# Kernel tuning notes

Measured on AMD Instinct MI355X. Metric: run time of the kernel, lower is better.

## Reference

```python
import jax, jax.numpy as jnp
import numpy as np

N_NODES = 16384
N_EDGES = 8192
D_FEAT = 64


def setup_inputs() -> dict:
    key = jax.random.key(0)
    k1, k2 = jax.random.split(key)
    incidence_matrix = jax.random.uniform(k1, (N_NODES, N_EDGES), dtype=jnp.float32)
    features = jax.random.normal(k2, (N_NODES, D_FEAT), dtype=jnp.float32)
    return {"incidence_matrix": incidence_matrix, "features": features}


def reference(incidence_matrix, features):
    # Faithful to the original: compute_degree_matrices returns RAW degree
    # diagonals (no inversion despite variable names). torch.diag(d) @ X is
    # exactly a row-broadcast scaling d[:, None] * X.
    d_v = jnp.sum(incidence_matrix, axis=1)  # [N] node degrees
    d_e = jnp.sum(incidence_matrix, axis=0)  # [M] hyperedge degrees
    X = features * d_v[:, None]                       # D_v @ X        [N, d]
    X_hyperedge = incidence_matrix.T @ X              # H^T @ X        [M, d]
    X_hyperedge = X_hyperedge * d_e[:, None]          # D_e @ (.)      [M, d]
    X = incidence_matrix @ X_hyperedge                # H @ (.)        [N, d]
    X = X * d_v[:, None]                              # D_v @ (.)      [N, d]
    return X
```

## Files before the change

kernel.cpp:

```cpp
#include <hip/hip_runtime.h>

#define N_NODES 16384
#define N_EDGES 8192
#define D_FEAT  64


__global__ __launch_bounds__(256, 4) void dvscale_kernel(const float* __restrict__ H,
                                                         const float* __restrict__ F,
                                                         float* __restrict__ dv,
                                                         float* __restrict__ Xs) {
    const int wave = threadIdx.x >> 6;
    const int lane = threadIdx.x & 63;
    const int n = blockIdx.x * 4 + wave;
    const float4* row = (const float4*)(H + (size_t)n * N_EDGES);
    float s = 0.f;
#pragma unroll
    for (int j = 0; j < 32; ++j) {
        float4 v = row[lane + 64 * j];
        s += v.x + v.y + v.z + v.w;
    }
#pragma unroll
    for (int off = 32; off > 0; off >>= 1) s += __shfl_down(s, off, 64);
    s = __shfl(s, 0, 64);
    if (lane == 0) dv[n] = s;
    Xs[(size_t)n * D_FEAT + lane] = F[(size_t)n * D_FEAT + lane] * s;
}

__global__ __launch_bounds__(256, 4) void gemm1_kernel(const float* __restrict__ H,
                                                       const float* __restrict__ Xs,
                                                       float* __restrict__ Y,
                                                       float* __restrict__ de) {
    const int et = blockIdx.x & 127;
    const int ks = blockIdx.x >> 7;
    const int e0 = et * 64;
    const int kbeg = ks * 2048;
    const int kend = kbeg + 2048;

    __shared__ float Hs[32 * 68];
    __shared__ float Xt[32 * 68];

    const int t = threadIdx.x;
    const int r  = t >> 4;
    const int c4 = (t & 15) * 4;
    const int eg = (t & 15) * 4;
    const int dg = (t >> 4) * 4;

    float acc[4][4] = {};
    float dea[4] = {0.f, 0.f, 0.f, 0.f};

    for (int k0 = kbeg; k0 < kend; k0 += 32) {
        __syncthreads();
#pragma unroll
        for (int i = 0; i < 2; ++i) {
            const int rr = r + 16 * i;
            float4 h = *(const float4*)(H + (size_t)(k0 + rr) * N_EDGES + e0 + c4);
            *(float4*)(Hs + rr * 68 + c4) = h;
            dea[0] += h.x; dea[1] += h.y; dea[2] += h.z; dea[3] += h.w;
            float4 x = *(const float4*)(Xs + (size_t)(k0 + rr) * D_FEAT + c4);
            *(float4*)(Xt + rr * 68 + c4) = x;
        }
        __syncthreads();
#pragma unroll 8
        for (int k = 0; k < 32; ++k) {
            float4 h = *(const float4*)(Hs + k * 68 + eg);
            float4 x = *(const float4*)(Xt + k * 68 + dg);
            acc[0][0] += h.x * x.x; acc[0][1] += h.x * x.y; acc[0][2] += h.x * x.z; acc[0][3] += h.x * x.w;
            acc[1][0] += h.y * x.x; acc[1][1] += h.y * x.y; acc[1][2] += h.y * x.z; acc[1][3] += h.y * x.w;
            acc[2][0] += h.z * x.x; acc[2][1] += h.z * x.y; acc[2][2] += h.z * x.z; acc[2][3] += h.z * x.w;
            acc[3][0] += h.w * x.x; acc[3][1] += h.w * x.y; acc[3][2] += h.w * x.z; acc[3][3] += h.w * x.w;
        }
    }

#pragma unroll
    for (int i = 0; i < 4; ++i)
#pragma unroll
        for (int j = 0; j < 4; ++j)
            atomicAdd(&Y[(size_t)(e0 + eg + i) * D_FEAT + dg + j], acc[i][j]);
#pragma unroll
    for (int j = 0; j < 4; ++j) atomicAdd(&de[e0 + c4 + j], dea[j]);
}

__global__ __launch_bounds__(256) void scaley_kernel(float* __restrict__ Y,
                                                     const float* __restrict__ de) {
    const int idx = blockIdx.x * 256 + threadIdx.x;
    const int e = idx >> 4;
    const float d = de[e];
    float4 v = ((float4*)Y)[idx];
    v.x *= d; v.y *= d; v.z *= d; v.w *= d;
    ((float4*)Y)[idx] = v;
}

__global__ __launch_bounds__(256, 4) void gemm2_kernel(const float* __restrict__ H,
                                                       const float* __restrict__ Y,
                                                       float* __restrict__ Yacc) {
    const int mt = blockIdx.x & 255;
    const int ks = blockIdx.x >> 8;
    const int m0 = mt * 64;
    const int kbeg = ks * 2048;
    const int kend = kbeg + 2048;

    __shared__ float Hst[32 * 68];
    __shared__ float Yt[32 * 68];

    const int t = threadIdx.x;
    const int mg = (t & 15) * 4;
    const int dg = (t >> 4) * 4;

    float acc[4][4] = {};

    for (int k0 = kbeg; k0 < kend; k0 += 32) {
        __syncthreads();
#pragma unroll
        for (int i = 0; i < 2; ++i) {
            const int idx = t + 256 * i;
            const int m = idx >> 3;
            const int k4 = (idx & 7) * 4;
            float4 h = *(const float4*)(H + (size_t)(m0 + m) * N_EDGES + k0 + k4);
            Hst[(k4 + 0) * 68 + m] = h.x;
            Hst[(k4 + 1) * 68 + m] = h.y;
            Hst[(k4 + 2) * 68 + m] = h.z;
            Hst[(k4 + 3) * 68 + m] = h.w;
            const int rr = idx >> 4;
            const int c4 = (idx & 15) * 4;
            float4 y = *(const float4*)(Y + (size_t)(k0 + rr) * D_FEAT + c4);
            *(float4*)(Yt + rr * 68 + c4) = y;
        }
        __syncthreads();
#pragma unroll 8
        for (int k = 0; k < 32; ++k) {
            float4 h = *(const float4*)(Hst + k * 68 + mg);
            float4 x = *(const float4*)(Yt + k * 68 + dg);
            acc[0][0] += h.x * x.x; acc[0][1] += h.x * x.y; acc[0][2] += h.x * x.z; acc[0][3] += h.x * x.w;
            acc[1][0] += h.y * x.x; acc[1][1] += h.y * x.y; acc[1][2] += h.y * x.z; acc[1][3] += h.y * x.w;
            acc[2][0] += h.z * x.x; acc[2][1] += h.z * x.y; acc[2][2] += h.z * x.z; acc[2][3] += h.z * x.w;
            acc[3][0] += h.w * x.x; acc[3][1] += h.w * x.y; acc[3][2] += h.w * x.z; acc[3][3] += h.w * x.w;
        }
    }

#pragma unroll
    for (int i = 0; i < 4; ++i)
#pragma unroll
        for (int j = 0; j < 4; ++j)
            atomicAdd(&Yacc[(size_t)(m0 + mg + i) * D_FEAT + dg + j], acc[i][j]);
}

__global__ __launch_bounds__(256) void scaleout_kernel(const float* __restrict__ Yacc,
                                                       const float* __restrict__ dv,
                                                       float* __restrict__ out) {
    const int idx = blockIdx.x * 256 + threadIdx.x;
    const int n = idx >> 4;
    const float d = dv[n];
    float4 v = ((const float4*)Yacc)[idx];
    v.x *= d; v.y *= d; v.z *= d; v.w *= d;
    ((float4*)out)[idx] = v;
}

extern "C" void kernel_launch(void* const* d_in, const int* in_sizes, int n_in,
                              void* d_out, int out_size, void* d_ws, size_t ws_size,
                              hipStream_t stream) {
    const float* H = (const float*)d_in[0];
    const float* F = (const float*)d_in[1];
    float* out = (float*)d_out;
    float* ws = (float*)d_ws;

    float* dv   = ws;
    float* de   = ws + 16384;
    float* Xs   = ws + 24576;
    float* Y    = ws + 24576 + N_NODES * D_FEAT;
    float* Yacc = Y + N_EDGES * D_FEAT;

    hipMemsetAsync(de, 0, N_EDGES * sizeof(float), stream);
    hipMemsetAsync(Y, 0, (size_t)N_EDGES * D_FEAT * sizeof(float), stream);
    hipMemsetAsync(Yacc, 0, (size_t)N_NODES * D_FEAT * sizeof(float), stream);

    dvscale_kernel<<<N_NODES / 4, 256, 0, stream>>>(H, F, dv, Xs);
    gemm1_kernel<<<1024, 256, 0, stream>>>(H, Xs, Y, de);
    scaley_kernel<<<(N_EDGES * D_FEAT / 4) / 256, 256, 0, stream>>>(Y, de);
    gemm2_kernel<<<1024, 256, 0, stream>>>(H, Y, Yacc);
    scaleout_kernel<<<(N_NODES * D_FEAT / 4) / 256, 256, 0, stream>>>(Yacc, dv, out);
}
```

Baseline: 1.228 ms.

## Convert H to bf16 once and run both GEMMs on bf16 MFMA

The degree pass now also writes a bf16 copy of the incidence matrix. Both GEMMs then read this half-size copy and use MFMA 16x16x32 bf16 instructions with swizzled LDS tiles, replacing the fp32 FMA loops. A transpose kernel makes the scaled features and the intermediate K-contiguous bf16, so the MFMA operands can be loaded directly. This removes fp32 scalar compute and halves H traffic in the GEMMs, at the cost of one extra bf16 write of H and a loss of precision that could exceed the harness tolerance. The edge degrees are now summed from the bf16-rounded values.

```diff
diff --git a/kernel.cpp b/kernel.cpp
--- a/kernel.cpp
+++ b/kernel.cpp
@@ -4,20 +4,38 @@
 #define N_EDGES 8192
 #define D_FEAT  64
 
-
-__global__ __launch_bounds__(256, 4) void dvscale_kernel(const float* __restrict__ H,
-                                                         const float* __restrict__ F,
-                                                         float* __restrict__ dv,
-                                                         float* __restrict__ Xs) {
+typedef __attribute__((ext_vector_type(8))) short short8;
+typedef __attribute__((ext_vector_type(4))) float floatx4;
+
+__device__ __forceinline__ unsigned short f2bf(float f) {
+    unsigned int u = __float_as_uint(f);
+    return (unsigned short)((u + 0x7fffu + ((u >> 16) & 1u)) >> 16);
+}
+
+__device__ __forceinline__ int sw(int row, int g) {
+    return row * 32 + (g ^ (((row >> 3) & 7) * 4));
+}
+
+__global__ __launch_bounds__(256) void dvscale_kernel(const float* __restrict__ H,
+                                                      const float* __restrict__ F,
+                                                      float* __restrict__ dv,
+                                                      unsigned short* __restrict__ Hbf,
+                                                      float* __restrict__ Xs) {
     const int wave = threadIdx.x >> 6;
     const int lane = threadIdx.x & 63;
     const int n = blockIdx.x * 4 + wave;
     const float4* row = (const float4*)(H + (size_t)n * N_EDGES);
+    unsigned short* hrow = Hbf + (size_t)n * N_EDGES;
     float s = 0.f;
 #pragma unroll
     for (int j = 0; j < 32; ++j) {
         float4 v = row[lane + 64 * j];
         s += v.x + v.y + v.z + v.w;
+        unsigned long long pk = (unsigned long long)f2bf(v.x)
+                              | ((unsigned long long)f2bf(v.y) << 16)
+                              | ((unsigned long long)f2bf(v.z) << 32)
+                              | ((unsigned long long)f2bf(v.w) << 48);
+        *(unsigned long long*)(hrow + 4 * (lane + 64 * j)) = pk;
     }
 #pragma unroll
     for (int off = 32; off > 0; off >>= 1) s += __shfl_down(s, off, 64);
@@ -26,131 +44,207 @@
     Xs[(size_t)n * D_FEAT + lane] = F[(size_t)n * D_FEAT + lane] * s;
 }
 
-__global__ __launch_bounds__(256, 4) void gemm1_kernel(const float* __restrict__ H,
-                                                       const float* __restrict__ Xs,
-                                                       float* __restrict__ Y,
-                                                       float* __restrict__ de) {
-    const int et = blockIdx.x & 127;
-    const int ks = blockIdx.x >> 7;
-    const int e0 = et * 64;
-    const int kbeg = ks * 2048;
-    const int kend = kbeg + 2048;
-
-    __shared__ float Hs[32 * 68];
-    __shared__ float Xt[32 * 68];
-
+__global__ __launch_bounds__(256) void xst_kernel(const float* __restrict__ Xs,
+                                                  unsigned short* __restrict__ XsT) {
+    __shared__ float tile[64][65];
+    const int n0 = blockIdx.x * 64;
     const int t = threadIdx.x;
-    const int r  = t >> 4;
-    const int c4 = (t & 15) * 4;
-    const int eg = (t & 15) * 4;
-    const int dg = (t >> 4) * 4;
-
-    float acc[4][4] = {};
-    float dea[4] = {0.f, 0.f, 0.f, 0.f};
-
-    for (int k0 = kbeg; k0 < kend; k0 += 32) {
-        __syncthreads();
-#pragma unroll
-        for (int i = 0; i < 2; ++i) {
-            const int rr = r + 16 * i;
-            float4 h = *(const float4*)(H + (size_t)(k0 + rr) * N_EDGES + e0 + c4);
-            *(float4*)(Hs + rr * 68 + c4) = h;
-            dea[0] += h.x; dea[1] += h.y; dea[2] += h.z; dea[3] += h.w;
-            float4 x = *(const float4*)(Xs + (size_t)(k0 + rr) * D_FEAT + c4);
-            *(float4*)(Xt + rr * 68 + c4) = x;
-        }
-        __syncthreads();
-#pragma unroll 8
-        for (int k = 0; k < 32; ++k) {
-            float4 h = *(const float4*)(Hs + k * 68 + eg);
-            float4 x = *(const float4*)(Xt + k * 68 + dg);
-            acc[0][0] += h.x * x.x; acc[0][1] += h.x * x.y; acc[0][2] += h.x * x.z; acc[0][3] += h.x * x.w;
-            acc[1][0] += h.y * x.x; acc[1][1] += h.y * x.y; acc[1][2] += h.y * x.z; acc[1][3] += h.y * x.w;
-            acc[2][0] += h.z * x.x; acc[2][1] += h.z * x.y; acc[2][2] += h.z * x.z; acc[2][3] += h.z * x.w;
-            acc[3][0] += h.w * x.x; acc[3][1] += h.w * x.y; acc[3][2] += h.w * x.z; acc[3][3] += h.w * x.w;
-        }
-    }
-
-#pragma unroll
-    for (int i = 0; i < 4; ++i)
+    const int r = t >> 4, c4 = t & 15;
+#pragma unroll
+    for (int li = 0; li < 4; ++li) {
+        const int rr = r + 16 * li;
+        float4 v = *(const float4*)(Xs + (size_t)(n0 + rr) * 64 + c4 * 4);
+        tile[rr][c4 * 4 + 0] = v.x; tile[rr][c4 * 4 + 1] = v.y;
+        tile[rr][c4 * 4 + 2] = v.z; tile[rr][c4 * 4 + 3] = v.w;
+    }
+    __syncthreads();
+#pragma unroll
+    for (int li = 0; li < 4; ++li) {
+        const int d = r + 16 * li;
+        unsigned long long pk = (unsigned long long)f2bf(tile[c4 * 4 + 0][d])
+                              | ((unsigned long long)f2bf(tile[c4 * 4 + 1][d]) << 16)
+                              | ((unsigned long long)f2bf(tile[c4 * 4 + 2][d]) << 32)
+                              | ((unsigned long long)f2bf(tile[c4 * 4 + 3][d]) << 48);
+        *(unsigned long long*)(XsT + (size_t)d * N_NODES + n0 + c4 * 4) = pk;
+    }
+}
+
+__global__ __launch_bounds__(256) void gemm1_kernel(const unsigned short* __restrict__ Hbf,
+                                                    const unsigned short* __restrict__ XsT,
+                                                    float* __restrict__ YaccT,
+                                                    float* __restrict__ de) {
+    __shared__ unsigned int A32[128 * 32];
+    __shared__ unsigned int B32[64 * 32];
+    const int t = threadIdx.x;
+    const int w = t >> 6;
+    const int lane = t & 63;
+    const int e0 = (blockIdx.x & 63) * 128;
+    const int k0base = (blockIdx.x >> 6) * 1024;
+
+    const int seg = t & 15;
+    const int p = t >> 4;
+    const int bd = t >> 3;
+    const int bseg = t & 7;
+
+    floatx4 acc[2][4];
+#pragma unroll
+    for (int i = 0; i < 2; ++i)
+#pragma unroll
+        for (int j = 0; j < 4; ++j) acc[i][j] = (floatx4){0.f, 0.f, 0.f, 0.f};
+    float dea[8] = {0.f, 0.f, 0.f, 0.f, 0.f, 0.f, 0.f, 0.f};
+
+    for (int it = 0; it < 16; ++it) {
+        const int k0 = k0base + it * 64;
+        __syncthreads();
+#pragma unroll
+        for (int pp = 0; pp < 2; ++pp) {
+            const int pr = p + 16 * pp;
+            const unsigned short* src = Hbf + (size_t)(k0 + 2 * pr) * N_EDGES + e0 + seg * 8;
+            short8 r0 = *(const short8*)src;
+            short8 r1 = *(const short8*)(src + N_EDGES);
+#pragma unroll
+            for (int j = 0; j < 8; ++j) {
+                unsigned int lo = (unsigned short)r0[j];
+                unsigned int hi = (unsigned short)r1[j];
+                unsigned int pk = lo | (hi << 16);
+                const int e = seg * 8 + j;
+                A32[sw(e, pr & ~3) + (pr & 3)] = pk;
+                dea[j] += __uint_as_float(pk << 16) + __uint_as_float(pk & 0xffff0000u);
+            }
+        }
+#pragma unroll
+        for (int bb = 0; bb < 2; ++bb) {
+            const int d = bd + 32 * bb;
+            uint4 v = *(const uint4*)(XsT + (size_t)d * N_NODES + k0 + bseg * 8);
+            *(uint4*)&B32[sw(d, bseg * 4)] = v;
+        }
+        __syncthreads();
+#pragma unroll
+        for (int s = 0; s < 2; ++s) {
+            const int g = s * 16 + (lane >> 4) * 4;
+            short8 af[2];
+#pragma unroll
+            for (int i = 0; i < 2; ++i) {
+                const int row = 32 * w + 16 * i + (lane & 15);
+                af[i] = *(short8*)&A32[sw(row, g)];
+            }
+#pragma unroll
+            for (int j = 0; j < 4; ++j) {
+                const int row = 16 * j + (lane & 15);
+                short8 bf = *(short8*)&B32[sw(row, g)];
+#pragma unroll
+                for (int i = 0; i < 2; ++i)
+                    acc[i][j] = __builtin_amdgcn_mfma_f32_16x16x32_bf16(af[i], bf, acc[i][j], 0, 0, 0);
+            }
+        }
+    }
+
+#pragma unroll
+    for (int i = 0; i < 2; ++i)
 #pragma unroll
         for (int j = 0; j < 4; ++j)
-            atomicAdd(&Y[(size_t)(e0 + eg + i) * D_FEAT + dg + j], acc[i][j]);
-#pragma unroll
-    for (int j = 0; j < 4; ++j) atomicAdd(&de[e0 + c4 + j], dea[j]);
-}
-
-__global__ __launch_bounds__(256) void scaley_kernel(float* __restrict__ Y,
-                                                     const float* __restrict__ de) {
+#pragma unroll
+            for (int r = 0; r < 4; ++r) {
+                const int e = e0 + 32 * w + 16 * i + (lane >> 4) * 4 + r;
+                const int d = 16 * j + (lane & 15);
+                atomicAdd(&YaccT[(size_t)d * N_EDGES + e], acc[i][j][r]);
+            }
+#pragma unroll
+    for (int j = 0; j < 8; ++j) atomicAdd(&de[e0 + seg * 8 + j], dea[j]);
+}
+
+__global__ __launch_bounds__(256) void scaley_kernel(const float* __restrict__ YaccT,
+                                                     const float* __restrict__ de,
+                                                     unsigned short* __restrict__ Yt) {
     const int idx = blockIdx.x * 256 + threadIdx.x;
-    const int e = idx >> 4;
-    const float d = de[e];
-    float4 v = ((float4*)Y)[idx];
-    v.x *= d; v.y *= d; v.z *= d; v.w *= d;
-    ((float4*)Y)[idx] = v;
-}
-
-__global__ __launch_bounds__(256, 4) void gemm2_kernel(const float* __restrict__ H,
-                                                       const float* __restrict__ Y,
-                                                       float* __restrict__ Yacc) {
-    const int mt = blockIdx.x & 255;
-    const int ks = blockIdx.x >> 8;
-    const int m0 = mt * 64;
-    const int kbeg = ks * 2048;
-    const int kend = kbeg + 2048;
-
-    __shared__ float Hst[32 * 68];
-    __shared__ float Yt[32 * 68];
-
+    const int d = idx >> 11;
+    const int e4 = idx & 2047;
+    float4 y = ((const float4*)YaccT)[idx];
+    float4 sc = ((const float4*)de)[e4];
+    unsigned long long pk = (unsigned long long)f2bf(y.x * sc.x)
+                          | ((unsigned long long)f2bf(y.y * sc.y) << 16)
+                          | ((unsigned long long)f2bf(y.z * sc.z) << 32)
+                          | ((unsigned long long)f2bf(y.w * sc.w) << 48);
+    *(unsigned long long*)(Yt + (size_t)d * N_EDGES + e4 * 4) = pk;
+}
+
+__global__ __launch_bounds__(256) void gemm2_kernel(const unsigned short* __restrict__ Hbf,
+                                                    const unsigned short* __restrict__ Yt,
+                                                    float* __restrict__ OutAcc) {
+    __shared__ unsigned int A32[128 * 32];
+    __shared__ unsigned int B32[64 * 32];
     const int t = threadIdx.x;
-    const int mg = (t & 15) * 4;
-    const int dg = (t >> 4) * 4;
-
-    float acc[4][4] = {};
-
-    for (int k0 = kbeg; k0 < kend; k0 += 32) {
-        __syncthreads();
-#pragma unroll
-        for (int i = 0; i < 2; ++i) {
-            const int idx = t + 256 * i;
-            const int m = idx >> 3;
-            const int k4 = (idx & 7) * 4;
-            float4 h = *(const float4*)(H + (size_t)(m0 + m) * N_EDGES + k0 + k4);
-            Hst[(k4 + 0) * 68 + m] = h.x;
-            Hst[(k4 + 1) * 68 + m] = h.y;
-            Hst[(k4 + 2) * 68 + m] = h.z;
-            Hst[(k4 + 3) * 68 + m] = h.w;
-            const int rr = idx >> 4;
-            const int c4 = (idx & 15) * 4;
-            float4 y = *(const float4*)(Y + (size_t)(k0 + rr) * D_FEAT + c4);
-            *(float4*)(Yt + rr * 68 + c4) = y;
-        }
-        __syncthreads();
-#pragma unroll 8
-        for (int k = 0; k < 32; ++k) {
-            float4 h = *(const float4*)(Hst + k * 68 + mg);
-            float4 x = *(const float4*)(Yt + k * 68 + dg);
-            acc[0][0] += h.x * x.x; acc[0][1] += h.x * x.y; acc[0][2] += h.x * x.z; acc[0][3] += h.x * x.w;
-            acc[1][0] += h.y * x.x; acc[1][1] += h.y * x.y; acc[1][2] += h.y * x.z; acc[1][3] += h.y * x.w;
-            acc[2][0] += h.z * x.x; acc[2][1] += h.z * x.y; acc[2][2] += h.z * x.z; acc[2][3] += h.z * x.w;
-            acc[3][0] += h.w * x.x; acc[3][1] += h.w * x.y; acc[3][2] += h.w * x.z; acc[3][3] += h.w * x.w;
-        }
-    }
-
-#pragma unroll
-    for (int i = 0; i < 4; ++i)
+    const int w = t >> 6;
+    const int lane = t & 63;
+    const int m0 = (blockIdx.x & 127) * 128;
+    const int k0base = (blockIdx.x >> 7) * 1024;
+
+    const int aseg = t & 7;
+    const int am = t >> 3;
+    const int bd = t >> 3;
+    const int bseg = t & 7;
+
+    floatx4 acc[2][4];
+#pragma unroll
+    for (int i = 0; i < 2; ++i)
+#pragma unroll
+        for (int j = 0; j < 4; ++j) acc[i][j] = (floatx4){0.f, 0.f, 0.f, 0.f};
+
+    for (int it = 0; it < 16; ++it) {
+        const int k0 = k0base + it * 64;
+        __syncthreads();
+#pragma unroll
+        for (int li = 0; li < 4; ++li) {
+            const int m = am + 32 * li;
+            uint4 v = *(const uint4*)(Hbf + (size_t)(m0 + m) * N_EDGES + k0 + aseg * 8);
+            *(uint4*)&A32[sw(m, aseg * 4)] = v;
+        }
+#pragma unroll
+        for (int bb = 0; bb < 2; ++bb) {
+            const int d = bd + 32 * bb;
+            uint4 v = *(const uint4*)(Yt + (size_t)d * N_EDGES + k0 + bseg * 8);
+            *(uint4*)&B32[sw(d, bseg * 4)] = v;
+        }
+        __syncthreads();
+#pragma unroll
+        for (int s = 0; s < 2; ++s) {
+            const int g = s * 16 + (lane >> 4) * 4;
+            short8 af[2];
+#pragma unroll
+            for (int i = 0; i < 2; ++i) {
+                const int row = 32 * w + 16 * i + (lane & 15);
+                af[i] = *(short8*)&A32[sw(row, g)];
+            }
+#pragma unroll
+            for (int j = 0; j < 4; ++j) {
+                const int row = 16 * j + (lane & 15);
+                short8 bf = *(short8*)&B32[sw(row, g)];
+#pragma unroll
+                for (int i = 0; i < 2; ++i)
+                    acc[i][j] = __builtin_amdgcn_mfma_f32_16x16x32_bf16(af[i], bf, acc[i][j], 0, 0, 0);
+            }
+        }
+    }
+
+#pragma unroll
+    for (int i = 0; i < 2; ++i)
 #pragma unroll
         for (int j = 0; j < 4; ++j)
-            atomicAdd(&Yacc[(size_t)(m0 + mg + i) * D_FEAT + dg + j], acc[i][j]);
-}
-
-__global__ __launch_bounds__(256) void scaleout_kernel(const float* __restrict__ Yacc,
+#pragma unroll
+            for (int r = 0; r < 4; ++r) {
+                const int n = m0 + 32 * w + 16 * i + (lane >> 4) * 4 + r;
+                const int d = 16 * j + (lane & 15);
+                atomicAdd(&OutAcc[(size_t)n * D_FEAT + d], acc[i][j][r]);
+            }
+}
+
+__global__ __launch_bounds__(256) void scaleout_kernel(const float* __restrict__ OutAcc,
                                                        const float* __restrict__ dv,
                                                        float* __restrict__ out) {
     const int idx = blockIdx.x * 256 + threadIdx.x;
     const int n = idx >> 4;
     const float d = dv[n];
-    float4 v = ((const float4*)Yacc)[idx];
+    float4 v = ((const float4*)OutAcc)[idx];
     v.x *= d; v.y *= d; v.z *= d; v.w *= d;
     ((float4*)out)[idx] = v;
 }
@@ -161,21 +255,25 @@
     const float* H = (const float*)d_in[0];
     const float* F = (const float*)d_in[1];
     float* out = (float*)d_out;
-    float* ws = (float*)d_ws;
-
-    float* dv   = ws;
-    float* de   = ws + 16384;
-    float* Xs   = ws + 24576;
-    float* Y    = ws + 24576 + N_NODES * D_FEAT;
-    float* Yacc = Y + N_EDGES * D_FEAT;
+    char* base = (char*)d_ws;
+
+    float* dv = (float*)base;
+    float* de = (float*)(base + 65536);
+    float* Xs = (float*)(base + 98304);
+    float* YaccT = (float*)(base + 98304 + 4194304);
+    float* OutAcc = (float*)(base + 98304 + 4194304 + 2097152);
+    unsigned short* XsT = (unsigned short*)(base + 98304 + 4194304 + 2097152 + 4194304);
+    unsigned short* Yt = XsT + (size_t)64 * N_NODES;
+    unsigned short* Hbf = (unsigned short*)((char*)Yt + 1048576);
 
     hipMemsetAsync(de, 0, N_EDGES * sizeof(float), stream);
-    hipMemsetAsync(Y, 0, (size_t)N_EDGES * D_FEAT * sizeof(float), stream);
-    hipMemsetAsync(Yacc, 0, (size_t)N_NODES * D_FEAT * sizeof(float), stream);
-
-    dvscale_kernel<<<N_NODES / 4, 256, 0, stream>>>(H, F, dv, Xs);
-    gemm1_kernel<<<1024, 256, 0, stream>>>(H, Xs, Y, de);
-    scaley_kernel<<<(N_EDGES * D_FEAT / 4) / 256, 256, 0, stream>>>(Y, de);
-    gemm2_kernel<<<1024, 256, 0, stream>>>(H, Y, Yacc);
-    scaleout_kernel<<<(N_NODES * D_FEAT / 4) / 256, 256, 0, stream>>>(Yacc, dv, out);
-}
+    hipMemsetAsync(YaccT, 0, (size_t)64 * N_EDGES * sizeof(float), stream);
+    hipMemsetAsync(OutAcc, 0, (size_t)N_NODES * D_FEAT * sizeof(float), stream);
+
+    dvscale_kernel<<<N_NODES / 4, 256, 0, stream>>>(H, F, dv, Hbf, Xs);
+    xst_kernel<<<N_NODES / 64, 256, 0, stream>>>(Xs, XsT);
+    gemm1_kernel<<<1024, 256, 0, stream>>>(Hbf, XsT, YaccT, de);
+    scaley_kernel<<<512, 256, 0, stream>>>(YaccT, de, Yt);
+    gemm2_kernel<<<1024, 256, 0, stream>>>(Hbf, Yt, OutAcc);
+    scaleout_kernel<<<1024, 256, 0, stream>>>(OutAcc, dv, out);
+}
```

Result: faster. 1.008 ms (-17.9%).
